# Performance work log

Hardware: AMD Instinct MI355X
Metric: run time of the kernel (lower is better)

The kernel has to match this reference:

```python
import jax, jax.numpy as jnp
import numpy as np

NUM_HEADS = 8
DIM = 512
B, S = 4, 2048
EPS = 1e-6


def _mha(x, wq, bq, wk, bk, wv, bv, wo, bo):
    # x: [B,S,D]; standard multi-head self-attention (tfa MultiHeadAttention math)
    Bx, Sx, D = x.shape
    hd = D // NUM_HEADS
    q = (x @ wq + bq).reshape(Bx, Sx, NUM_HEADS, hd)
    k = (x @ wk + bk).reshape(Bx, Sx, NUM_HEADS, hd)
    v = (x @ wv + bv).reshape(Bx, Sx, NUM_HEADS, hd)
    scores = jnp.einsum('bqhd,bkhd->bhqk', q, k) / jnp.sqrt(jnp.asarray(hd, x.dtype))
    attn = jax.nn.softmax(scores, axis=-1)
    out = jnp.einsum('bhqk,bkhd->bqhd', attn, v).reshape(Bx, Sx, D)
    return out @ wo + bo


def _ln(x, g, b):
    m = jnp.mean(x, axis=-1, keepdims=True)
    v = jnp.mean((x - m) ** 2, axis=-1, keepdims=True)
    return (x - m) * jax.lax.rsqrt(v + EPS) * g + b


def setup_inputs() -> dict:
    key = jax.random.key(0)
    ks = jax.random.split(key, 32)
    D, F = DIM, 4 * DIM
    std = 0.02
    def w(k, shape):
        return jax.random.normal(k, shape, dtype=jnp.float32) * std
    inp = {'x': jax.random.normal(ks[0], (B, S, D), dtype=jnp.float32)}
    # temporal attention params
    for i, nm in enumerate(['t', 's']):
        base = 1 + i * 8
        inp[nm + '_wq'] = w(ks[base + 0], (D, D)); inp[nm + '_bq'] = jnp.zeros((D,), jnp.float32)
        inp[nm + '_wk'] = w(ks[base + 1], (D, D)); inp[nm + '_bk'] = jnp.zeros((D,), jnp.float32)
        inp[nm + '_wv'] = w(ks[base + 2], (D, D)); inp[nm + '_bv'] = jnp.zeros((D,), jnp.float32)
        inp[nm + '_wo'] = w(ks[base + 3], (D, D)); inp[nm + '_bo'] = jnp.zeros((D,), jnp.float32)
    inp['ln1_g'] = jnp.ones((D,), jnp.float32); inp['ln1_b'] = jnp.zeros((D,), jnp.float32)
    inp['ln2_g'] = jnp.ones((D,), jnp.float32); inp['ln2_b'] = jnp.zeros((D,), jnp.float32)
    inp['f_w1'] = w(ks[20], (D, F)); inp['f_b1'] = jnp.zeros((F,), jnp.float32)
    inp['f_w2'] = w(ks[21], (F, D)); inp['f_b2'] = jnp.zeros((D,), jnp.float32)
    return inp


def reference(x,
              t_wq, t_bq, t_wk, t_bk, t_wv, t_bv, t_wo, t_bo,
              s_wq, s_bq, s_wk, s_bk, s_wv, s_bv, s_wo, s_bo,
              ln1_g, ln1_b, ln2_g, ln2_b,
              f_w1, f_b1, f_w2, f_b2):
    temporal = _mha(x, t_wq, t_bq, t_wk, t_bk, t_wv, t_bv, t_wo, t_bo)
    h = _ln(x + temporal, ln1_g, ln1_b)
    spatial = _mha(h, s_wq, s_bq, s_wk, s_bk, s_wv, s_bv, s_wo, s_bo)
    h2 = _ln(h + spatial, ln2_g, ln2_b)
    ffn = jax.nn.gelu(h2 @ f_w1 + f_b1, approximate=False) @ f_w2 + f_b2
    return h2 + ffn
```

## Files before the change

kernel.cpp:

```cpp
#include <hip/hip_runtime.h>

typedef __bf16 bf16x8 __attribute__((ext_vector_type(8)));
typedef float  f32x4  __attribute__((ext_vector_type(4)));

#define DEVI static __device__ __forceinline__

DEVI __bf16 tobf(float f) { return static_cast<__bf16>(f); }

__global__ __launch_bounds__(256) void cast_f32_bf16(
    const float* __restrict__ in, __bf16* __restrict__ out, int n8)
{
  int i = blockIdx.x * 256 + threadIdx.x;
  if (i >= n8) return;
  const float4* p = (const float4*)in + (size_t)i * 2;
  float4 a = p[0], b = p[1];
  bf16x8 o;
  o[0]=tobf(a.x); o[1]=tobf(a.y); o[2]=tobf(a.z); o[3]=tobf(a.w);
  o[4]=tobf(b.x); o[5]=tobf(b.y); o[6]=tobf(b.z); o[7]=tobf(b.w);
  ((bf16x8*)out)[i] = o;
}

__global__ __launch_bounds__(256) void transpose_cast(
    const float* __restrict__ W, __bf16* __restrict__ Wt, int R, int C)
{
  __shared__ float tile[32][33];
  const int tx = threadIdx.x & 31;
  const int ty = threadIdx.x >> 5;
  const int c0 = blockIdx.x * 32, r0 = blockIdx.y * 32;
  #pragma unroll
  for (int i = 0; i < 4; ++i)
    tile[ty + i*8][tx] = W[(size_t)(r0 + ty + i*8) * C + c0 + tx];
  __syncthreads();
  #pragma unroll
  for (int i = 0; i < 4; ++i)
    Wt[(size_t)(c0 + ty + i*8) * R + r0 + tx] = tobf(tile[tx][ty + i*8]);
}

__global__ __launch_bounds__(256) void concat3(
    const float* __restrict__ a, const float* __restrict__ b,
    const float* __restrict__ c, float* __restrict__ out, int n)
{
  int i = blockIdx.x * 256 + threadIdx.x;
  if (i < n) out[i] = a[i];
  else if (i < 2*n) out[i] = b[i - n];
  else if (i < 3*n) out[i] = c[i - 2*n];
}

template<int EPI>
__global__ __launch_bounds__(256)
void gemm_bt(const __bf16* __restrict__ A, const __bf16* __restrict__ Bt,
             const float* __restrict__ bias, const float* __restrict__ resid,
             void* __restrict__ out, int M, int N, int K)
{
  __shared__ __bf16 As[128][72];
  __shared__ __bf16 Bs[128][72];
  const int tid  = threadIdx.x;
  const int lane = tid & 63;
  const int wave = tid >> 6;
  const int wm = wave >> 1, wn = wave & 1;
  const int m0 = blockIdx.x * 128, n0 = blockIdx.y * 128;
  const int lr = lane & 15, lg = lane >> 4;
  const int srow = tid >> 3, scol = (tid & 7) * 8;

  f32x4 acc[4][4];
  f32x4 zz = {0.f, 0.f, 0.f, 0.f};
  #pragma unroll
  for (int i = 0; i < 4; ++i)
    #pragma unroll
    for (int j = 0; j < 4; ++j) acc[i][j] = zz;

  for (int k0 = 0; k0 < K; k0 += 64) {
    #pragma unroll
    for (int p = 0; p < 4; ++p) {
      const int row = p * 32 + srow;
      *(bf16x8*)&As[row][scol] = *(const bf16x8*)(A  + (size_t)(m0 + row) * K + k0 + scol);
      *(bf16x8*)&Bs[row][scol] = *(const bf16x8*)(Bt + (size_t)(n0 + row) * K + k0 + scol);
    }
    __syncthreads();
    #pragma unroll
    for (int kk = 0; kk < 2; ++kk) {
      bf16x8 af[4], bfr[4];
      #pragma unroll
      for (int i = 0; i < 4; ++i) af[i]  = *(const bf16x8*)&As[wm*64 + i*16 + lr][kk*32 + lg*8];
      #pragma unroll
      for (int j = 0; j < 4; ++j) bfr[j] = *(const bf16x8*)&Bs[wn*64 + j*16 + lr][kk*32 + lg*8];
      #pragma unroll
      for (int i = 0; i < 4; ++i)
        #pragma unroll
        for (int j = 0; j < 4; ++j)
          acc[i][j] = __builtin_amdgcn_mfma_f32_16x16x32_bf16(af[i], bfr[j], acc[i][j], 0, 0, 0);
    }
    __syncthreads();
  }

  const int orow = m0 + wm * 64;
  const int ocol = n0 + wn * 64;
  #pragma unroll
  for (int j = 0; j < 4; ++j) {
    const int col = ocol + j*16 + lr;
    const float bv = bias[col];
    #pragma unroll
    for (int i = 0; i < 4; ++i) {
      #pragma unroll
      for (int r = 0; r < 4; ++r) {
        const int row = orow + i*16 + lg*4 + r;
        const size_t o = (size_t)row * N + col;
        float v = acc[i][j][r] + bv;
        if (EPI == 0) {
          ((__bf16*)out)[o] = tobf(v);
        } else if (EPI == 1) {
          float g = 0.5f * v * (1.0f + erff(v * 0.7071067811865476f));
          ((__bf16*)out)[o] = tobf(g);
        } else {
          ((float*)out)[o] = v + resid[o];
        }
      }
    }
  }
}

DEVI int vt_idx(int d, int kv) {
  return d * 72 + ((((kv >> 3) + (d >> 3)) & 7) << 3) + (kv & 7);
}

__global__ __launch_bounds__(256)
void flash_attn(const __bf16* __restrict__ QKV, __bf16* __restrict__ O)
{
  __shared__ __bf16 Qs[64][72];
  __shared__ __bf16 Ks[64][72];
  __shared__ __bf16 VTs[64 * 72];
  __shared__ __bf16 Ps[4][16][72];

  const int tid  = threadIdx.x;
  const int lane = tid & 63;
  const int w    = tid >> 6;
  const int lr = lane & 15, lg = lane >> 4;
  const int bh = blockIdx.y;
  const int b = bh >> 3, h = bh & 7;
  const int q0 = blockIdx.x * 64;
  const size_t qkvbase = (size_t)b * 2048 * 1536 + h * 64;
  const int srow = tid >> 3, scol = (tid & 7) * 8;

  #pragma unroll
  for (int p = 0; p < 2; ++p) {
    const int row = p * 32 + srow;
    *(bf16x8*)&Qs[row][scol] = *(const bf16x8*)(QKV + qkvbase + (size_t)(q0 + row) * 1536 + scol);
  }

  float mrow[4], lrow[4];
  f32x4 oacc[4];
  f32x4 zz = {0.f, 0.f, 0.f, 0.f};
  #pragma unroll
  for (int r = 0; r < 4; ++r) { mrow[r] = -1e30f; lrow[r] = 0.f; }
  #pragma unroll
  for (int d = 0; d < 4; ++d) oacc[d] = zz;

  for (int kt = 0; kt < 32; ++kt) {
    const size_t kbase = qkvbase + 512  + (size_t)(kt * 64) * 1536;
    const size_t vbase = qkvbase + 1024 + (size_t)(kt * 64) * 1536;
    #pragma unroll
    for (int p = 0; p < 2; ++p) {
      const int row = p * 32 + srow;
      *(bf16x8*)&Ks[row][scol] = *(const bf16x8*)(QKV + kbase + (size_t)row * 1536 + scol);
      bf16x8 vv = *(const bf16x8*)(QKV + vbase + (size_t)row * 1536 + scol);
      #pragma unroll
      for (int e = 0; e < 8; ++e) VTs[vt_idx(scol + e, row)] = vv[e];
    }
    __syncthreads();

    f32x4 sf[4];
    #pragma unroll
    for (int ct = 0; ct < 4; ++ct) {
      f32x4 s = zz;
      #pragma unroll
      for (int kk = 0; kk < 2; ++kk) {
        bf16x8 a  = *(const bf16x8*)&Qs[w*16 + lr][kk*32 + lg*8];
        bf16x8 bb = *(const bf16x8*)&Ks[ct*16 + lr][kk*32 + lg*8];
        s = __builtin_amdgcn_mfma_f32_16x16x32_bf16(a, bb, s, 0, 0, 0);
      }
      #pragma unroll
      for (int e = 0; e < 4; ++e) sf[ct][e] = s[e] * 0.125f;
    }

    #pragma unroll
    for (int r = 0; r < 4; ++r) {
      float tmax = fmaxf(fmaxf(sf[0][r], sf[1][r]), fmaxf(sf[2][r], sf[3][r]));
      #pragma unroll
      for (int off = 1; off < 16; off <<= 1) tmax = fmaxf(tmax, __shfl_xor(tmax, off));
      const float mnew = fmaxf(mrow[r], tmax);
      const float sc = __expf(mrow[r] - mnew);
      float psum = 0.f;
      #pragma unroll
      for (int ct = 0; ct < 4; ++ct) {
        float pv = __expf(sf[ct][r] - mnew);
        sf[ct][r] = pv;
        psum += pv;
      }
      #pragma unroll
      for (int off = 1; off < 16; off <<= 1) psum += __shfl_xor(psum, off);
      lrow[r] = lrow[r] * sc + psum;
      mrow[r] = mnew;
      #pragma unroll
      for (int d = 0; d < 4; ++d) oacc[d][r] *= sc;
    }

    #pragma unroll
    for (int ct = 0; ct < 4; ++ct)
      #pragma unroll
      for (int r = 0; r < 4; ++r)
        Ps[w][lg*4 + r][ct*16 + lr] = tobf(sf[ct][r]);

    #pragma unroll
    for (int dt = 0; dt < 4; ++dt) {
      #pragma unroll
      for (int kk = 0; kk < 2; ++kk) {
        bf16x8 a  = *(const bf16x8*)&Ps[w][lr][kk*32 + lg*8];
        bf16x8 bb = *(const bf16x8*)&VTs[vt_idx(dt*16 + lr, kk*32 + lg*8)];
        oacc[dt] = __builtin_amdgcn_mfma_f32_16x16x32_bf16(a, bb, oacc[dt], 0, 0, 0);
      }
    }
    __syncthreads();
  }

  float linv[4];
  #pragma unroll
  for (int r = 0; r < 4; ++r) linv[r] = 1.0f / lrow[r];
  #pragma unroll
  for (int dt = 0; dt < 4; ++dt)
    #pragma unroll
    for (int r = 0; r < 4; ++r) {
      const int row = q0 + w*16 + lg*4 + r;
      O[(size_t)(b * 2048 + row) * 512 + h*64 + dt*16 + lr] = tobf(oacc[dt][r] * linv[r]);
    }
}

__global__ __launch_bounds__(256)
void ln_kernel(const float* __restrict__ in, const float* __restrict__ gw,
               const float* __restrict__ bw, float* __restrict__ outF,
               __bf16* __restrict__ outB)
{
  const int lane = threadIdx.x & 63;
  const size_t row = (size_t)blockIdx.x * 4 + (threadIdx.x >> 6);
  const float* p = in + row * 512 + lane * 8;
  float4 v0 = *(const float4*)p;
  float4 v1 = *(const float4*)(p + 4);
  float s = (v0.x + v0.y) + (v0.z + v0.w) + (v1.x + v1.y) + (v1.z + v1.w);
  float q = v0.x*v0.x + v0.y*v0.y + v0.z*v0.z + v0.w*v0.w
          + v1.x*v1.x + v1.y*v1.y + v1.z*v1.z + v1.w*v1.w;
  #pragma unroll
  for (int off = 1; off < 64; off <<= 1) { s += __shfl_xor(s, off); q += __shfl_xor(q, off); }
  const float mean = s * (1.0f / 512.0f);
  const float var  = q * (1.0f / 512.0f) - mean * mean;
  const float rs   = rsqrtf(var + 1e-6f);
  const float4 g0 = *(const float4*)(gw + lane * 8);
  const float4 g1 = *(const float4*)(gw + lane * 8 + 4);
  const float4 b0 = *(const float4*)(bw + lane * 8);
  const float4 b1 = *(const float4*)(bw + lane * 8 + 4);
  float4 o0, o1;
  o0.x = (v0.x - mean) * rs * g0.x + b0.x;
  o0.y = (v0.y - mean) * rs * g0.y + b0.y;
  o0.z = (v0.z - mean) * rs * g0.z + b0.z;
  o0.w = (v0.w - mean) * rs * g0.w + b0.w;
  o1.x = (v1.x - mean) * rs * g1.x + b1.x;
  o1.y = (v1.y - mean) * rs * g1.y + b1.y;
  o1.z = (v1.z - mean) * rs * g1.z + b1.z;
  o1.w = (v1.w - mean) * rs * g1.w + b1.w;
  *(float4*)(outF + row * 512 + lane * 8)     = o0;
  *(float4*)(outF + row * 512 + lane * 8 + 4) = o1;
  bf16x8 ob;
  ob[0]=tobf(o0.x); ob[1]=tobf(o0.y); ob[2]=tobf(o0.z); ob[3]=tobf(o0.w);
  ob[4]=tobf(o1.x); ob[5]=tobf(o1.y); ob[6]=tobf(o1.z); ob[7]=tobf(o1.w);
  *(bf16x8*)(outB + row * 512 + lane * 8) = ob;
}

extern "C" void kernel_launch(void* const* d_in, const int* in_sizes, int n_in,
                              void* d_out, int out_size, void* d_ws, size_t ws_size,
                              hipStream_t stream)
{
  const float* x     = (const float*)d_in[0];
  const float* t_wq  = (const float*)d_in[1];
  const float* t_bq  = (const float*)d_in[2];
  const float* t_wk  = (const float*)d_in[3];
  const float* t_bk  = (const float*)d_in[4];
  const float* t_wv  = (const float*)d_in[5];
  const float* t_bv  = (const float*)d_in[6];
  const float* t_wo  = (const float*)d_in[7];
  const float* t_bo  = (const float*)d_in[8];
  const float* s_wq  = (const float*)d_in[9];
  const float* s_bq  = (const float*)d_in[10];
  const float* s_wk  = (const float*)d_in[11];
  const float* s_bk  = (const float*)d_in[12];
  const float* s_wv  = (const float*)d_in[13];
  const float* s_bv  = (const float*)d_in[14];
  const float* s_wo  = (const float*)d_in[15];
  const float* s_bo  = (const float*)d_in[16];
  const float* ln1_g = (const float*)d_in[17];
  const float* ln1_b = (const float*)d_in[18];
  const float* ln2_g = (const float*)d_in[19];
  const float* ln2_b = (const float*)d_in[20];
  const float* f_w1  = (const float*)d_in[21];
  const float* f_b1  = (const float*)d_in[22];
  const float* f_w2  = (const float*)d_in[23];
  const float* f_b2  = (const float*)d_in[24];

  char* ws = (char*)d_ws;
  size_t off = 0;
  auto alloc = [&](size_t bytes) -> void* {
    void* p = ws + off; off += (bytes + 255) & ~(size_t)255; return p;
  };

  __bf16* qkvb  = (__bf16*)alloc(8192ull * 1536 * 2);
  __bf16* attnb = (__bf16*)alloc(8192ull * 512 * 2);
  __bf16* gelu_b = qkvb;
  __bf16* xb    = (__bf16*)alloc(8192ull * 512 * 2);
  __bf16* h_bf  = xb;
  __bf16* wT_t  = (__bf16*)alloc(1536ull * 512 * 2);
  __bf16* wT_s  = (__bf16*)alloc(1536ull * 512 * 2);
  __bf16* woT_t = (__bf16*)alloc(512ull * 512 * 2);
  __bf16* woT_s = (__bf16*)alloc(512ull * 512 * 2);
  __bf16* w1T   = (__bf16*)alloc(2048ull * 512 * 2);
  __bf16* w2T   = (__bf16*)alloc(512ull * 2048 * 2);
  float* bcat_t = (float*)alloc(1536 * 4);
  float* bcat_s = (float*)alloc(1536 * 4);
  float* tmp_f  = (float*)alloc(8192ull * 512 * 4);
  float* h_f    = (float*)alloc(8192ull * 512 * 4);
  float* h2_f   = (float*)alloc(8192ull * 512 * 4);
  __bf16* h2_bf = (__bf16*)alloc(8192ull * 512 * 2);
  (void)in_sizes; (void)n_in; (void)out_size; (void)ws_size;

  cast_f32_bf16<<<2048, 256, 0, stream>>>(x, xb, 524288);
  transpose_cast<<<dim3(16,16), 256, 0, stream>>>(t_wq, wT_t,               512, 512);
  transpose_cast<<<dim3(16,16), 256, 0, stream>>>(t_wk, wT_t + 512*512,     512, 512);
  transpose_cast<<<dim3(16,16), 256, 0, stream>>>(t_wv, wT_t + 2*512*512,   512, 512);
  transpose_cast<<<dim3(16,16), 256, 0, stream>>>(s_wq, wT_s,               512, 512);
  transpose_cast<<<dim3(16,16), 256, 0, stream>>>(s_wk, wT_s + 512*512,     512, 512);
  transpose_cast<<<dim3(16,16), 256, 0, stream>>>(s_wv, wT_s + 2*512*512,   512, 512);
  transpose_cast<<<dim3(16,16), 256, 0, stream>>>(t_wo, woT_t,              512, 512);
  transpose_cast<<<dim3(16,16), 256, 0, stream>>>(s_wo, woT_s,              512, 512);
  transpose_cast<<<dim3(64,16), 256, 0, stream>>>(f_w1, w1T,                512, 2048);
  transpose_cast<<<dim3(16,64), 256, 0, stream>>>(f_w2, w2T,                2048, 512);
  concat3<<<6, 256, 0, stream>>>(t_bq, t_bk, t_bv, bcat_t, 512);
  concat3<<<6, 256, 0, stream>>>(s_bq, s_bk, s_bv, bcat_s, 512);

  gemm_bt<0><<<dim3(64,12), 256, 0, stream>>>(xb, wT_t, bcat_t, nullptr, qkvb, 8192, 1536, 512);
  flash_attn<<<dim3(32,32), 256, 0, stream>>>(qkvb, attnb);
  gemm_bt<2><<<dim3(64,4),  256, 0, stream>>>(attnb, woT_t, t_bo, x, tmp_f, 8192, 512, 512);
  ln_kernel<<<2048, 256, 0, stream>>>(tmp_f, ln1_g, ln1_b, h_f, h_bf);

  gemm_bt<0><<<dim3(64,12), 256, 0, stream>>>(h_bf, wT_s, bcat_s, nullptr, qkvb, 8192, 1536, 512);
  flash_attn<<<dim3(32,32), 256, 0, stream>>>(qkvb, attnb);
  gemm_bt<2><<<dim3(64,4),  256, 0, stream>>>(attnb, woT_s, s_bo, h_f, tmp_f, 8192, 512, 512);
  ln_kernel<<<2048, 256, 0, stream>>>(tmp_f, ln2_g, ln2_b, h2_f, h2_bf);

  gemm_bt<1><<<dim3(64,16), 256, 0, stream>>>(h2_bf, w1T, f_b1, nullptr, gelu_b, 8192, 2048, 512);
  gemm_bt<2><<<dim3(64,4),  256, 0, stream>>>(gelu_b, w2T, f_b2, h2_f, (float*)d_out, 8192, 512, 2048);
}
```

Measured before the change: 582.9 us.

## Pre-transpose V, keep scaled Q in registers, XOR-swizzle attention LDS

Adds a separate kernel that writes V transposed per head to global memory, so flash attention loads V^T tiles with vector stores instead of scattering elements into shared memory. Q fragments are loaded once into registers with the 1/8 scale applied up front, which removes the Q shared tile and the per-score multiply. K, V^T and P tiles use an XOR-swizzled 128-byte row layout to avoid LDS bank conflicts, and s_setprio is raised around the MFMA sections. This costs an extra kernel launch, an extra global round trip for V, and pre-scaling Q in bf16 adds a small rounding difference.

```diff
diff --git a/kernel.cpp b/kernel.cpp
--- a/kernel.cpp
+++ b/kernel.cpp
@@ -44,6 +44,32 @@
   if (i < n) out[i] = a[i];
   else if (i < 2*n) out[i] = b[i - n];
   else if (i < 3*n) out[i] = c[i - 2*n];
+}
+
+__global__ __launch_bounds__(256)
+void transpose_v(const __bf16* __restrict__ QKV, __bf16* __restrict__ VT)
+{
+  __shared__ __bf16 t[64][72];
+  const int tid = threadIdx.x;
+  const int bh = blockIdx.y;
+  const int b = bh >> 3, h = bh & 7;
+  const int s0 = blockIdx.x * 64;
+  const int srow = tid >> 3, scol = (tid & 7) * 8;
+  #pragma unroll
+  for (int p = 0; p < 2; ++p) {
+    const int row = srow + p * 32;
+    *(bf16x8*)&t[row][scol] =
+      *(const bf16x8*)(QKV + (size_t)(b * 2048 + s0 + row) * 1536 + 1024 + h * 64 + scol);
+  }
+  __syncthreads();
+  #pragma unroll
+  for (int p = 0; p < 2; ++p) {
+    const int d = srow + p * 32;
+    bf16x8 v;
+    #pragma unroll
+    for (int e = 0; e < 8; ++e) v[e] = t[scol + e][d];
+    *(bf16x8*)(VT + ((size_t)bh * 64 + d) * 2048 + s0 + scol) = v;
+  }
 }
 
 template<int EPI>
@@ -119,17 +145,17 @@
   }
 }
 
-DEVI int vt_idx(int d, int kv) {
-  return d * 72 + ((((kv >> 3) + (d >> 3)) & 7) << 3) + (kv & 7);
+DEVI int sw_off(int row, int colByte) {
+  return row * 128 + (colByte ^ ((row & 7) << 4));
 }
 
 __global__ __launch_bounds__(256)
-void flash_attn(const __bf16* __restrict__ QKV, __bf16* __restrict__ O)
-{
-  __shared__ __bf16 Qs[64][72];
-  __shared__ __bf16 Ks[64][72];
-  __shared__ __bf16 VTs[64 * 72];
-  __shared__ __bf16 Ps[4][16][72];
+void flash_attn(const __bf16* __restrict__ QKV, const __bf16* __restrict__ VT,
+                __bf16* __restrict__ O)
+{
+  __shared__ __align__(16) char Ks [64 * 128];
+  __shared__ __align__(16) char VTs[64 * 128];
+  __shared__ __align__(16) char Ps [4 * 16 * 128];
 
   const int tid  = threadIdx.x;
   const int lane = tid & 63;
@@ -139,12 +165,17 @@
   const int b = bh >> 3, h = bh & 7;
   const int q0 = blockIdx.x * 64;
   const size_t qkvbase = (size_t)b * 2048 * 1536 + h * 64;
+  const size_t vtbase  = (size_t)bh * 64 * 2048;
   const int srow = tid >> 3, scol = (tid & 7) * 8;
 
-  #pragma unroll
-  for (int p = 0; p < 2; ++p) {
-    const int row = p * 32 + srow;
-    *(bf16x8*)&Qs[row][scol] = *(const bf16x8*)(QKV + qkvbase + (size_t)(q0 + row) * 1536 + scol);
+  bf16x8 aq[2];
+  #pragma unroll
+  for (int kk = 0; kk < 2; ++kk) {
+    bf16x8 t = *(const bf16x8*)(QKV + qkvbase +
+                 (size_t)(q0 + w*16 + lr) * 1536 + kk*32 + lg*8);
+    #pragma unroll
+    for (int e = 0; e < 8; ++e) t[e] = tobf(0.125f * (float)t[e]);
+    aq[kk] = t;
   }
 
   float mrow[4], lrow[4];
@@ -156,31 +187,30 @@
   for (int d = 0; d < 4; ++d) oacc[d] = zz;
 
   for (int kt = 0; kt < 32; ++kt) {
-    const size_t kbase = qkvbase + 512  + (size_t)(kt * 64) * 1536;
-    const size_t vbase = qkvbase + 1024 + (size_t)(kt * 64) * 1536;
+    const size_t kbase = qkvbase + 512 + (size_t)(kt * 64) * 1536;
     #pragma unroll
     for (int p = 0; p < 2; ++p) {
-      const int row = p * 32 + srow;
-      *(bf16x8*)&Ks[row][scol] = *(const bf16x8*)(QKV + kbase + (size_t)row * 1536 + scol);
-      bf16x8 vv = *(const bf16x8*)(QKV + vbase + (size_t)row * 1536 + scol);
-      #pragma unroll
-      for (int e = 0; e < 8; ++e) VTs[vt_idx(scol + e, row)] = vv[e];
+      const int row = srow + p * 32;
+      *(bf16x8*)(Ks  + sw_off(row, scol * 2)) =
+        *(const bf16x8*)(QKV + kbase + (size_t)row * 1536 + scol);
+      *(bf16x8*)(VTs + sw_off(row, scol * 2)) =
+        *(const bf16x8*)(VT + vtbase + (size_t)row * 2048 + kt * 64 + scol);
     }
     __syncthreads();
 
     f32x4 sf[4];
+    __builtin_amdgcn_s_setprio(1);
     #pragma unroll
     for (int ct = 0; ct < 4; ++ct) {
       f32x4 s = zz;
       #pragma unroll
       for (int kk = 0; kk < 2; ++kk) {
-        bf16x8 a  = *(const bf16x8*)&Qs[w*16 + lr][kk*32 + lg*8];
-        bf16x8 bb = *(const bf16x8*)&Ks[ct*16 + lr][kk*32 + lg*8];
-        s = __builtin_amdgcn_mfma_f32_16x16x32_bf16(a, bb, s, 0, 0, 0);
+        bf16x8 bb = *(const bf16x8*)(Ks + sw_off(ct*16 + lr, kk*64 + lg*16));
+        s = __builtin_amdgcn_mfma_f32_16x16x32_bf16(aq[kk], bb, s, 0, 0, 0);
       }
-      #pragma unroll
-      for (int e = 0; e < 4; ++e) sf[ct][e] = s[e] * 0.125f;
-    }
+      sf[ct] = s;
+    }
+    __builtin_amdgcn_s_setprio(0);
 
     #pragma unroll
     for (int r = 0; r < 4; ++r) {
@@ -208,17 +238,19 @@
     for (int ct = 0; ct < 4; ++ct)
       #pragma unroll
       for (int r = 0; r < 4; ++r)
-        Ps[w][lg*4 + r][ct*16 + lr] = tobf(sf[ct][r]);
-
+        *(__bf16*)(Ps + w*2048 + sw_off(lg*4 + r, (ct*16 + lr) * 2)) = tobf(sf[ct][r]);
+
+    __builtin_amdgcn_s_setprio(1);
     #pragma unroll
     for (int dt = 0; dt < 4; ++dt) {
       #pragma unroll
       for (int kk = 0; kk < 2; ++kk) {
-        bf16x8 a  = *(const bf16x8*)&Ps[w][lr][kk*32 + lg*8];
-        bf16x8 bb = *(const bf16x8*)&VTs[vt_idx(dt*16 + lr, kk*32 + lg*8)];
+        bf16x8 a  = *(const bf16x8*)(Ps  + w*2048 + sw_off(lr, kk*64 + lg*16));
+        bf16x8 bb = *(const bf16x8*)(VTs + sw_off(dt*16 + lr, kk*64 + lg*16));
         oacc[dt] = __builtin_amdgcn_mfma_f32_16x16x32_bf16(a, bb, oacc[dt], 0, 0, 0);
       }
     }
+    __builtin_amdgcn_s_setprio(0);
     __syncthreads();
   }
 
@@ -314,6 +346,7 @@
   __bf16* gelu_b = qkvb;
   __bf16* xb    = (__bf16*)alloc(8192ull * 512 * 2);
   __bf16* h_bf  = xb;
+  __bf16* vtb   = (__bf16*)alloc(8192ull * 512 * 2);
   __bf16* wT_t  = (__bf16*)alloc(1536ull * 512 * 2);
   __bf16* wT_s  = (__bf16*)alloc(1536ull * 512 * 2);
   __bf16* woT_t = (__bf16*)alloc(512ull * 512 * 2);
@@ -343,12 +376,14 @@
   concat3<<<6, 256, 0, stream>>>(s_bq, s_bk, s_bv, bcat_s, 512);
 
   gemm_bt<0><<<dim3(64,12), 256, 0, stream>>>(xb, wT_t, bcat_t, nullptr, qkvb, 8192, 1536, 512);
-  flash_attn<<<dim3(32,32), 256, 0, stream>>>(qkvb, attnb);
+  transpose_v<<<dim3(32,32), 256, 0, stream>>>(qkvb, vtb);
+  flash_attn<<<dim3(32,32), 256, 0, stream>>>(qkvb, vtb, attnb);
   gemm_bt<2><<<dim3(64,4),  256, 0, stream>>>(attnb, woT_t, t_bo, x, tmp_f, 8192, 512, 512);
   ln_kernel<<<2048, 256, 0, stream>>>(tmp_f, ln1_g, ln1_b, h_f, h_bf);
 
   gemm_bt<0><<<dim3(64,12), 256, 0, stream>>>(h_bf, wT_s, bcat_s, nullptr, qkvb, 8192, 1536, 512);
-  flash_attn<<<dim3(32,32), 256, 0, stream>>>(qkvb, attnb);
+  transpose_v<<<dim3(32,32), 256, 0, stream>>>(qkvb, vtb);
+  flash_attn<<<dim3(32,32), 256, 0, stream>>>(qkvb, vtb, attnb);
   gemm_bt<2><<<dim3(64,4),  256, 0, stream>>>(attnb, woT_s, s_bo, h_f, tmp_f, 8192, 512, 512);
   ln_kernel<<<2048, 256, 0, stream>>>(tmp_f, ln2_g, ln2_b, h2_f, h2_bf);
 
```

After: 534.9 us. -8.2%, faster.
